# Kernel optimization log

Hardware: AMD Instinct MI355X
Metric: run time of the kernel (lower is better)

Reference implementation:

```python
import jax, jax.numpy as jnp
import numpy as np
import math

N = 4096
E = 131072
IN_DIM, HID, OUT = 512, 256, 64
DEPTH = 3
RATIO = 0.5


def setup_inputs() -> dict:
    key = jax.random.key(0)
    ks = jax.random.split(key, 12)

    def w(k, fi, fo):
        return jax.random.normal(k, (fi, fo), jnp.float32) * (1.0 / np.sqrt(fi).astype(np.float32))

    return {
        "x": jax.random.normal(ks[0], (N, IN_DIM), jnp.float32),
        "edge_index": jax.random.randint(ks[1], (2, E), 0, N, jnp.int32),
        "dW0": w(ks[2], IN_DIM, HID), "dW1": w(ks[3], HID, HID),
        "dW2": w(ks[4], HID, HID), "dW3": w(ks[5], HID, HID),
        "db0": jnp.zeros((HID,), jnp.float32), "db1": jnp.zeros((HID,), jnp.float32),
        "db2": jnp.zeros((HID,), jnp.float32), "db3": jnp.zeros((HID,), jnp.float32),
        "pw0": jax.random.normal(ks[6], (HID,), jnp.float32),
        "pw1": jax.random.normal(ks[7], (HID,), jnp.float32),
        "pw2": jax.random.normal(ks[8], (HID,), jnp.float32),
        "uW0": w(ks[9], HID, HID), "uW1": w(ks[10], HID, HID), "uW2": w(ks[11], HID, OUT),
        "ub0": jnp.zeros((HID,), jnp.float32), "ub1": jnp.zeros((HID,), jnp.float32),
        "ub2": jnp.zeros((OUT,), jnp.float32),
    }


def gcn_conv(x, A, W, b):
    # GCNConv(improved=True): A_hat = A + 2I, sym-normalized.
    n = A.shape[0]
    eye = jnp.eye(n, dtype=A.dtype)
    Ah = A + 2.0 * eye
    d = Ah.sum(axis=1)
    dinv = jnp.where(d > 0, jax.lax.rsqrt(d), 0.0)
    An = dinv[:, None] * Ah * dinv[None, :]
    return An @ (x @ W) + b


def augment_adj(A):
    # add self loops, square the (weighted) adjacency, remove self loops
    n = A.shape[0]
    eye = jnp.eye(n, dtype=A.dtype)
    Al = A + eye
    A2 = Al @ Al
    return A2 * (1.0 - eye)


def topk_pool(x, A, w, k):
    # TopKPooling: score = tanh(x.w/||w||); keep top-k; gate kept features by score.
    score = jnp.tanh((x @ w) / jnp.linalg.norm(w))
    _, perm = jax.lax.top_k(score, k)
    xp = x[perm] * score[perm][:, None]
    return xp, A[perm][:, perm], perm


def _forward(x, edge_index, down_Ws, down_bs, pool_ws, up_Ws, up_bs):
    A = jnp.zeros((N, N), jnp.float32).at[edge_index[0], edge_index[1]].set(1.0)
    x = jax.nn.relu(gcn_conv(x, A, down_Ws[0], down_bs[0]))
    xs, As, perms = [x], [A], []
    n = N
    for i in range(1, DEPTH + 1):
        A = augment_adj(A)
        k = int(math.ceil(RATIO * n)); n = k
        x, A, perm = topk_pool(x, A, pool_ws[i - 1], k)
        x = jax.nn.relu(gcn_conv(x, A, down_Ws[i], down_bs[i]))
        if i < DEPTH:
            xs.append(x); As.append(A)
        perms.append(perm)
    for i in range(DEPTH):
        j = DEPTH - 1 - i
        res, A, perm = xs[j], As[j], perms[j]
        up = jnp.zeros_like(res).at[perm].set(x)   # unpool (sum_res=True)
        x = res + up
        x = gcn_conv(x, A, up_Ws[i], up_bs[i])
        if i < DEPTH - 1:
            x = jax.nn.relu(x)
    return x


def reference(x, edge_index, dW0, dW1, dW2, dW3, db0, db1, db2, db3,
              pw0, pw1, pw2, uW0, uW1, uW2, ub0, ub1, ub2):
    return _forward(x, edge_index,
                    [dW0, dW1, dW2, dW3], [db0, db1, db2, db3],
                    [pw0, pw1, pw2],
                    [uW0, uW1, uW2], [ub0, ub1, ub2])
```

## Files before the change

kernel.cpp:

```cpp
#include <hip/hip_runtime.h>
#include <math.h>

#define NN 4096
#define EE 131072
#define IN_DIM 512
#define HID 256
#define OUT_DIM 64
#define ECAP 128

typedef __attribute__((ext_vector_type(8))) short bf8_t;
typedef __attribute__((ext_vector_type(4))) float f4_t;
typedef __attribute__((ext_vector_type(8))) unsigned short us8_t;
typedef __attribute__((ext_vector_type(4))) unsigned short us4_t;

#define GAS __attribute__((address_space(1)))
#define LAS __attribute__((address_space(3)))

__device__ __forceinline__ unsigned short f2bf(float v){
  union { float f; unsigned u; } x; x.f = v;
  unsigned r = x.u + 0x7fffu + ((x.u >> 16) & 1u);
  return (unsigned short)(r >> 16);
}
__device__ __forceinline__ float bf2f(unsigned short h){
  union { float f; unsigned u; } x; x.u = ((unsigned)h) << 16;
  return x.f;
}

__device__ __forceinline__ float waveReduceSum(float v){
#pragma unroll
  for (int off = 32; off > 0; off >>= 1) v += __shfl_down(v, off);
  return v;
}

__global__ __launch_bounds__(256) void k_prep(
    const float* __restrict__ x_in, const float* __restrict__ dW0,
    const float* __restrict__ dW1, const float* __restrict__ dW2,
    const float* __restrict__ dW3, const float* __restrict__ uW0,
    const float* __restrict__ uW1, const float* __restrict__ uW2,
    unsigned* __restrict__ bits,
    unsigned short* __restrict__ xinh, unsigned short* __restrict__ xinl,
    unsigned short* __restrict__ W0th, unsigned short* __restrict__ W0tl,
    unsigned short* __restrict__ W5th, unsigned short* __restrict__ W5tl,
    unsigned short* __restrict__ W2th, unsigned short* __restrict__ W2tl)
{
  int b = blockIdx.x;
  if (b < 128){
    int base = b * 4096 + threadIdx.x;
#pragma unroll
    for (int i = 0; i < 16; ++i) bits[base + i * 256] = 0;
    return;
  }
  b -= 128;
  if (b < 2048){
    int i0 = b * 1024 + threadIdx.x;
#pragma unroll
    for (int i = 0; i < 4; ++i){
      int idx = i0 + i * 256;
      float v = x_in[idx];
      unsigned short h = f2bf(v);
      xinh[idx] = h; xinl[idx] = f2bf(v - bf2f(h));
    }
    return;
  }
  b -= 2048;
  const float* X; unsigned short *Th, *Tl; int R, C, tile;
  if (b < 128){ X = dW0; Th = W0th; Tl = W0tl; R = 512; C = 256; tile = b; }
  else if (b < 448){
    int t2 = b - 128; int z = t2 >> 6; int rem = t2 & 63;
    const float* ws[5] = {dW1, dW2, dW3, uW0, uW1};
    X = ws[z]; Th = W5th + (size_t)z * 65536; Tl = W5tl + (size_t)z * 65536;
    R = 256; C = 256; tile = rem;
  } else { X = uW2; Th = W2th; Tl = W2tl; R = 256; C = 64; tile = b - 448; }
  int tpr = C >> 5;
  int bx = (tile % tpr) * 32, by = (tile / tpr) * 32;
  __shared__ float t[32][33];
  int tx = threadIdx.x & 31, ty = threadIdx.x >> 5;
#pragma unroll
  for (int i = 0; i < 4; ++i)
    t[ty + i * 8][tx] = X[(size_t)(by + ty + i * 8) * C + bx + tx];
  __syncthreads();
#pragma unroll
  for (int i = 0; i < 4; ++i){
    float v = t[tx][ty + i * 8];
    unsigned short h = f2bf(v);
    size_t o = (size_t)(bx + ty + i * 8) * R + by + tx;
    Th[o] = h; Tl[o] = f2bf(v - bf2f(h));
  }
}

__global__ void k_build_bits(const int* __restrict__ ei, unsigned* __restrict__ bits){
  int e = blockIdx.x * blockDim.x + threadIdx.x;
  if (e < EE){
    int r = ei[e], c = ei[EE + e];
    atomicOr(&bits[r * 128 + (c >> 5)], 1u << (c & 31));
  }
}

__global__ __launch_bounds__(128) void k_ell(const unsigned* __restrict__ bits,
                                             int* __restrict__ ell, int* __restrict__ cnt,
                                             float* __restrict__ dinv){
  int r = blockIdx.x, t = threadIdx.x;
  unsigned w = bits[r * 128 + t];
  int c = __popc(w);
  __shared__ int sc[128];
  sc[t] = c; __syncthreads();
  for (int off = 1; off < 128; off <<= 1){
    int a = sc[t], b = (t >= off) ? sc[t - off] : 0;
    __syncthreads(); sc[t] = a + b; __syncthreads();
  }
  int total = sc[127];
  int pos = sc[t] - c;
  int base = r * ECAP;
  while (w){
    int b = __ffs(w) - 1; w &= w - 1;
    if (pos < ECAP) ell[base + pos] = t * 32 + b;
    pos++;
  }
  if (t == 0){
    cnt[r] = (total < ECAP) ? total : ECAP;
    dinv[r] = 1.0f / sqrtf((float)total + 2.0f);
  }
}

template<int NCOLS, int RELU, int SC>
__global__ __launch_bounds__(256) void k_spmm_ell(
    const int* __restrict__ ell, const int* __restrict__ cnt,
    const float* __restrict__ Zs, const float* __restrict__ dinv,
    const float* __restrict__ bias, float* __restrict__ out,
    const float* __restrict__ scw, float* __restrict__ score)
{
  int r = blockIdx.x;
  __shared__ int s_idx[ECAP];
  __shared__ int s_n;
  __shared__ float sh[4 * NCOLS];
  __shared__ float sd[4], sq[4];
  if (threadIdx.x == 0) s_n = cnt[r];
  __syncthreads();
  int n = s_n; if (n > ECAP) n = ECAP;
  for (int i = threadIdx.x; i < n; i += 256) s_idx[i] = ell[r * ECAP + i];
  __syncthreads();
  int wv = threadIdx.x >> 6, lane = threadIdx.x & 63;
  if (NCOLS == 256){
    f4_t acc = (f4_t){0.f, 0.f, 0.f, 0.f};
    for (int e = wv; e < n; e += 4){
      const f4_t* row = (const f4_t*)(Zs + (size_t)s_idx[e] * 256);
      acc += row[lane];
    }
    ((f4_t*)(sh + wv * 256))[lane] = acc;
  } else {
    float acc = 0.f;
    for (int e = wv; e < n; e += 4)
      acc += Zs[(size_t)s_idx[e] * 64 + lane];
    sh[wv * 64 + lane] = acc;
  }
  __syncthreads();
  int t = threadIdx.x;
  float o = 0.f;
  if (t < NCOLS){
    float y = sh[t] + sh[NCOLS + t] + sh[2 * NCOLS + t] + sh[3 * NCOLS + t];
    float z = Zs[(size_t)r * NCOLS + t];
    o = dinv[r] * (y + 2.0f * z) + bias[t];
    if (RELU) o = fmaxf(o, 0.f);
    out[(size_t)r * NCOLS + t] = o;
  }
  if (SC){
    float w = scw[t];
    float d = waveReduceSum(o * w);
    float q = waveReduceSum(w * w);
    if (!lane){ sd[wv] = d; sq[wv] = q; }
    __syncthreads();
    if (!t) score[r] = tanhf((sd[0] + sd[1] + sd[2] + sd[3]) / sqrtf(sq[0] + sq[1] + sq[2] + sq[3]));
  }
}

__global__ __launch_bounds__(256) void k_pool_build(
    const float* __restrict__ x0, const float* __restrict__ score,
    const int* __restrict__ perm1, const int* __restrict__ inv1,
    const int* __restrict__ ell, const int* __restrict__ cnt,
    unsigned short* __restrict__ xph, unsigned short* __restrict__ xpl,
    unsigned short* __restrict__ Rb2,
    unsigned short* __restrict__ xu1h, unsigned short* __restrict__ xu1l)
{
  int b = blockIdx.x;
  if (b < 2048){
    int pr = perm1[b]; float s = score[pr];
    int c = threadIdx.x;
    float v = x0[(size_t)pr * 256 + c] * s;
    unsigned short h = f2bf(v);
    xph[(size_t)b * 256 + c] = h;
    xpl[(size_t)b * 256 + c] = f2bf(v - bf2f(h));
    return;
  }
  if (b < 6144){
    int k = b - 2048;
    __shared__ unsigned char row[2048];
    for (int i = threadIdx.x; i < 512; i += 256) ((int*)row)[i] = 0;
    __syncthreads();
    int n = cnt[k];
    for (int e = threadIdx.x; e < n; e += 256){
      int s = inv1[ell[k * ECAP + e]];
      if (s >= 0) row[s] = 1;
    }
    __syncthreads();
    if (threadIdx.x == 0){
      int sk = inv1[k];
      if (sk >= 0) row[sk] += 1;
    }
    __syncthreads();
    unsigned w = 0;
#pragma unroll
    for (int j = 0; j < 8; ++j) w |= ((unsigned)row[(threadIdx.x << 3) + j]) << (2 * j);
    Rb2[k * 256 + threadIdx.x] = (unsigned short)w;
    return;
  }
  int r = b - 6144;
  if (inv1[r] < 0){
    int c = threadIdx.x;
    float v = x0[(size_t)r * 256 + c];
    unsigned short h = f2bf(v);
    xu1h[(size_t)r * 256 + c] = h;
    xu1l[(size_t)r * 256 + c] = f2bf(v - bf2f(h));
  }
}

template<int SRCL, int OUTL>
__global__ __launch_bounds__(256) void k_pp(
    const float* __restrict__ x, const float* __restrict__ score,
    const int* __restrict__ perm, const int* __restrict__ inv, int n, int k,
    unsigned short* __restrict__ xph, unsigned short* __restrict__ xpl,
    unsigned short* __restrict__ xuh, unsigned short* __restrict__ xul,
    const unsigned short* __restrict__ Ah, const unsigned short* __restrict__ Al,
    unsigned short* __restrict__ Lh, unsigned short* __restrict__ Ll,
    unsigned short* __restrict__ Rh, unsigned short* __restrict__ Rl)
{
  __shared__ float t[32][33];
  __shared__ int sinv[32];
  int b = blockIdx.x, c = threadIdx.x;
  if (b < k){
    int pr = perm[b]; float s = score[pr];
    float v = x[(size_t)pr * 256 + c] * s;
    unsigned short h = f2bf(v);
    xph[(size_t)b * 256 + c] = h;
    xpl[(size_t)b * 256 + c] = f2bf(v - bf2f(h));
    return;
  }
  b -= k;
  if (b < n){
    if (inv[b] < 0){
      float v = x[(size_t)b * 256 + c];
      unsigned short h = f2bf(v);
      xuh[(size_t)b * 256 + c] = h;
      xul[(size_t)b * 256 + c] = f2bf(v - bf2f(h));
    }
    return;
  }
  b -= n;
  if (b < k){
    int r = b, pr = perm[r];
    for (int cc = threadIdx.x; cc < n; cc += 256){
      float v = bf2f(Ah[(size_t)pr * n + cc]);
      if (SRCL) v += bf2f(Al[(size_t)pr * n + cc]);
      if (pr == cc) v += 1.f;
      unsigned short h = f2bf(v);
      Lh[(size_t)r * n + cc] = h;
      if (OUTL) Ll[(size_t)r * n + cc] = f2bf(v - bf2f(h));
    }
    return;
  }
  b -= k;
  int tpr = n >> 5;
  int kt = b / tpr, ct = b - kt * tpr;
  int tx = threadIdx.x & 31, ty = threadIdx.x >> 5;
  if (threadIdx.x < 32) sinv[threadIdx.x] = inv[ct * 32 + threadIdx.x];
#pragma unroll
  for (int i = 0; i < 4; ++i){
    int kl = ty + i * 8;
    size_t src = (size_t)(kt * 32 + kl) * n + ct * 32 + tx;
    float v = bf2f(Ah[src]);
    if (SRCL) v += bf2f(Al[src]);
    t[kl][tx] = v;
  }
  __syncthreads();
#pragma unroll
  for (int i = 0; i < 4; ++i){
    int cl = ty + i * 8;
    int s = sinv[cl];
    if (s >= 0){
      float v = t[tx][cl];
      if (kt * 32 + tx == ct * 32 + cl) v += 1.f;
      unsigned short h = f2bf(v);
      size_t o = (size_t)s * n + kt * 32 + tx;
      Rh[o] = h;
      if (OUTL) Rl[o] = f2bf(v - bf2f(h));
    }
  }
}

__global__ __launch_bounds__(256) void k_sq1(const int* __restrict__ ell, const int* __restrict__ cnt,
                                             const int* __restrict__ perm,
                                             const unsigned short* __restrict__ Rb2,
                                             unsigned short* __restrict__ A1h,
                                             float* __restrict__ dinv1){
  int r = blockIdx.x;
  int pr = perm[r];
  __shared__ int s_idx[ECAP];
  __shared__ int s_n;
  __shared__ float sred[4];
  if (threadIdx.x == 0) s_n = cnt[pr];
  for (int i = threadIdx.x; i < ECAP; i += 256) s_idx[i] = ell[pr * ECAP + i];
  __syncthreads();
  int n = s_n; if (n > ECAP) n = ECAP;
  int colb = threadIdx.x * 8;
  auto expand = [](unsigned x) -> uint2 {
    uint2 e;
    e.x = (x & 3) | (((x >> 2) & 3) << 8) | (((x >> 4) & 3) << 16) | (((x >> 6) & 3) << 24);
    e.y = ((x >> 8) & 3) | (((x >> 10) & 3) << 8) | (((x >> 12) & 3) << 16) | (((x >> 14) & 3) << 24);
    return e;
  };
  uint2 acc = expand(Rb2[pr * 256 + threadIdx.x]);
  for (int e = 0; e < n; ++e){
    uint2 v = expand(Rb2[s_idx[e] * 256 + threadIdx.x]);
    acc.x += v.x; acc.y += v.y;
  }
  float fs = 0.f;
  us8_t o;
#pragma unroll
  for (int j = 0; j < 8; ++j){
    unsigned byte = ((j < 4 ? acc.x : acc.y) >> (8 * (j & 3))) & 0xFFu;
    if (colb + j == r) byte = 0;
    float f = (float)byte;
    fs += f;
    o[j] = f2bf(f);
  }
  *(us8_t*)(A1h + (size_t)r * 2048 + colb) = o;
  fs = waveReduceSum(fs);
  int lane = threadIdx.x & 63, wd = threadIdx.x >> 6;
  if (!lane) sred[wd] = fs;
  __syncthreads();
  if (!threadIdx.x)
    dinv1[r] = 1.0f / sqrtf(sred[0] + sred[1] + sred[2] + sred[3] + 2.0f);
}

template<int HAS_AL, int HAS_BL, int HAS_LL, int EPI>
__global__ __launch_bounds__(256) void k_mm(
    const unsigned short* __restrict__ Ah, const unsigned short* __restrict__ Al,
    const unsigned short* __restrict__ Bh, const unsigned short* __restrict__ Bl,
    int M, int N, int K, int KS, float* __restrict__ P,
    float* __restrict__ Cf, unsigned short* __restrict__ Ch, unsigned short* __restrict__ Cl,
    const float* __restrict__ dinv)
{
  constexpr int NARR = 2 + HAS_AL + HAS_BL;
  constexpr int BUF = NARR * 8192;
  __shared__ int4 ldsq[NARR * 512 * 2];
  char* ldsc = (char*)ldsq;

  const int tid = threadIdx.x, lane = tid & 63, wid = tid >> 6;
  const int wm = wid >> 1, wn = wid & 1;
  const int nbx = gridDim.x, nby = gridDim.y;
  const int tot = nbx * nby * gridDim.z;
  int id = blockIdx.x + nbx * (blockIdx.y + nby * blockIdx.z);
  if ((tot & 7) == 0) id = (id & 7) * (tot >> 3) + (id >> 3);
  const int sx = id % nbx; int remq = id / nbx;
  const int sy = remq % nby;
  const int bm = sy << 6, bn = sx << 6;
  const int z = remq / nby;
  const int l15 = lane & 15, l4 = lane >> 4;

  f4_t acc[2][2];
#pragma unroll
  for (int i = 0; i < 2; ++i)
#pragma unroll
    for (int j = 0; j < 2; ++j) acc[i][j] = (f4_t){0.f, 0.f, 0.f, 0.f};

  const size_t rb = (size_t)K * 2;
  const size_t kz = (size_t)z * KS * 2;
  const char* pAh = (const char*)Ah + (size_t)bm * rb;
  const char* pAl = HAS_AL ? (const char*)Al + (size_t)bm * rb : nullptr;
  const char* pBh = (const char*)Bh + (size_t)bn * rb;
  const char* pBl = HAS_BL ? (const char*)Bl + (size_t)bn * rb : nullptr;

  auto stage = [&](int t, int b2){
    char* ldsb = ldsc + b2 * BUF;
    const size_t kb = kz + (size_t)t * 128;
#pragma unroll
    for (int it = 0; it < 2; ++it){
      const int idx = tid + (it << 8);
      const int row = idx >> 3;
      const int kc = ((idx & 7) << 4) ^ ((row & 7) << 4);
      const size_t go = (size_t)row * rb + kb + kc;
      const int lo = idx * 16;
      __builtin_amdgcn_global_load_lds((const GAS void*)(pAh + go), (LAS void*)(ldsb + lo), 16, 0, 0);
      __builtin_amdgcn_global_load_lds((const GAS void*)(pBh + go), (LAS void*)(ldsb + 8192 + lo), 16, 0, 0);
      if (HAS_AL)
        __builtin_amdgcn_global_load_lds((const GAS void*)(pAl + go), (LAS void*)(ldsb + 16384 + lo), 16, 0, 0);
      if (HAS_BL)
        __builtin_amdgcn_global_load_lds((const GAS void*)(pBl + go), (LAS void*)(ldsb + (2 + HAS_AL) * 8192 + lo), 16, 0, 0);
    }
  };

  const int T = KS >> 6;
  stage(0, 0);
  int b = 0;
  for (int t = 0; t < T; ++t){
    if (t + 1 < T){
      stage(t + 1, b ^ 1);
      if constexpr (NARR == 2) asm volatile("s_waitcnt vmcnt(4)" ::: "memory");
      else if constexpr (NARR == 3) asm volatile("s_waitcnt vmcnt(6)" ::: "memory");
      else asm volatile("s_waitcnt vmcnt(8)" ::: "memory");
    } else {
      asm volatile("s_waitcnt vmcnt(0)" ::: "memory");
    }
    __syncthreads();
    const char* ldsb = ldsc + b * BUF;
#pragma unroll
    for (int ks = 0; ks < 2; ++ks){
      bf8_t aH[2], aL[2], bH[2], bL[2];
#pragma unroll
      for (int f = 0; f < 2; ++f){
        int ar = wm * 32 + f * 16 + l15;
        int aoff = ar * 128 + (((ks * 64) + (l4 << 4)) ^ ((ar & 7) << 4));
        aH[f] = *(const bf8_t*)(ldsb + aoff);
        if (HAS_AL) aL[f] = *(const bf8_t*)(ldsb + 16384 + aoff);
        int br = wn * 32 + f * 16 + l15;
        int boff = br * 128 + (((ks * 64) + (l4 << 4)) ^ ((br & 7) << 4));
        bH[f] = *(const bf8_t*)(ldsb + 8192 + boff);
        if (HAS_BL) bL[f] = *(const bf8_t*)(ldsb + (2 + HAS_AL) * 8192 + boff);
      }
#pragma unroll
      for (int i = 0; i < 2; ++i)
#pragma unroll
        for (int j = 0; j < 2; ++j){
          acc[i][j] = __builtin_amdgcn_mfma_f32_16x16x32_bf16(aH[i], bH[j], acc[i][j], 0, 0, 0);
          if (HAS_BL) acc[i][j] = __builtin_amdgcn_mfma_f32_16x16x32_bf16(aH[i], bL[j], acc[i][j], 0, 0, 0);
          if (HAS_AL) acc[i][j] = __builtin_amdgcn_mfma_f32_16x16x32_bf16(aL[i], bH[j], acc[i][j], 0, 0, 0);
          if (HAS_LL) acc[i][j] = __builtin_amdgcn_mfma_f32_16x16x32_bf16(aL[i], bL[j], acc[i][j], 0, 0, 0);
        }
    }
    __syncthreads();
    b ^= 1;
  }

  if (EPI == 4){
    float* LT = (float*)ldsc;
#pragma unroll
    for (int i = 0; i < 2; ++i)
#pragma unroll
      for (int j = 0; j < 2; ++j)
#pragma unroll
        for (int r = 0; r < 4; ++r){
          int lr = wm * 32 + i * 16 + l4 * 4 + r;
          int lc = wn * 32 + j * 16 + l15;
          float sv = dinv[bm + lr] * acc[i][j][r];
          Cf[(size_t)(bm + lr) * N + bn + lc] = sv;
          LT[lr * 68 + lc] = sv;
        }
    __syncthreads();
    int col = tid >> 2;
    int seg = (tid & 3) << 4;
    us8_t h0, h1, l0, l1;
#pragma unroll
    for (int mm = 0; mm < 8; ++mm){
      float v = LT[(seg + mm) * 68 + col];
      unsigned short h = f2bf(v);
      h0[mm] = h; l0[mm] = f2bf(v - bf2f(h));
    }
#pragma unroll
    for (int mm = 0; mm < 8; ++mm){
      float v = LT[(seg + 8 + mm) * 68 + col];
      unsigned short h = f2bf(v);
      h1[mm] = h; l1[mm] = f2bf(v - bf2f(h));
    }
    size_t ob = (size_t)(bn + col) * M + bm + seg;
    *(us8_t*)(Ch + ob) = h0;
    *(us8_t*)(Ch + ob + 8) = h1;
    *(us8_t*)(Cl + ob) = l0;
    *(us8_t*)(Cl + ob + 8) = l1;
    return;
  }

  float* Pz = (EPI == 0) ? P + (size_t)z * M * N : nullptr;
#pragma unroll
  for (int i = 0; i < 2; ++i)
#pragma unroll
    for (int j = 0; j < 2; ++j)
#pragma unroll
      for (int r = 0; r < 4; ++r){
        int grow = bm + wm * 32 + i * 16 + l4 * 4 + r;
        int gcol = bn + wn * 32 + j * 16 + l15;
        float v = acc[i][j][r];
        size_t o = (size_t)grow * N + gcol;
        if (EPI == 0){
          Pz[o] = v;
        } else {
          Cf[o] = dinv[grow] * v;
        }
      }
}

template<int EPI, int SC, int Z>
__global__ __launch_bounds__(256) void k_red(
    const float* __restrict__ P, int M, int NC,
    const float* __restrict__ dinv, const float* __restrict__ Zs,
    const float* __restrict__ bias,
    float* __restrict__ Of, unsigned short* __restrict__ Oh, unsigned short* __restrict__ Ol,
    float* __restrict__ dout, int relu,
    const float* __restrict__ scw, float* __restrict__ score,
    const float* __restrict__ res, const int* __restrict__ permsel)
{
  int w = threadIdx.x >> 6, lane = threadIdx.x & 63;
  int row = blockIdx.x * 4 + w;
  int prow = (EPI == 4) ? permsel[row] : 0;
  float di = (EPI != 3) ? dinv[row] : 0.f;
  float rsum = 0.f, o_d = 0.f, o_q = 0.f;
  for (int c0 = lane * 4; c0 < NC; c0 += 256){
    size_t o = (size_t)row * NC + c0;
    f4_t s = *(const f4_t*)(P + o);
#pragma unroll
    for (int zz = 1; zz < Z; ++zz) s += *(const f4_t*)(P + (size_t)zz * M * NC + o);
    if (EPI == 2){
      f4_t z4 = *(const f4_t*)(Zs + o);
      f4_t b4 = *(const f4_t*)(bias + c0);
      f4_t out;
#pragma unroll
      for (int j = 0; j < 4; ++j){
        float v = di * (s[j] + 2.0f * z4[j]) + b4[j];
        if (relu) v = fmaxf(v, 0.f);
        out[j] = v;
      }
      *(f4_t*)(Of + o) = out;
      if (SC){
        f4_t w4 = *(const f4_t*)(scw + c0);
#pragma unroll
        for (int j = 0; j < 4; ++j){ o_d += out[j] * w4[j]; o_q += w4[j] * w4[j]; }
      }
    } else if (EPI == 3){
      us4_t h4, l4v;
#pragma unroll
      for (int j = 0; j < 4; ++j){
        float v = (c0 + j == row) ? 0.f : s[j];
        unsigned short h = f2bf(v);
        h4[j] = h; l4v[j] = f2bf(v - bf2f(h));
        rsum += v;
      }
      *(us4_t*)(Oh + o) = h4;
      *(us4_t*)(Ol + o) = l4v;
    } else {
      f4_t z4 = *(const f4_t*)(Zs + o);
      f4_t b4 = *(const f4_t*)(bias + c0);
      f4_t r4 = *(const f4_t*)(res + (size_t)prow * NC + c0);
      us4_t h4, l4v;
#pragma unroll
      for (int j = 0; j < 4; ++j){
        float v = di * (s[j] + 2.0f * z4[j]) + b4[j];
        if (relu) v = fmaxf(v, 0.f);
        float comb = r4[j] + v;
        unsigned short h = f2bf(comb);
        h4[j] = h; l4v[j] = f2bf(comb - bf2f(h));
      }
      size_t od = (size_t)prow * NC + c0;
      *(us4_t*)(Oh + od) = h4;
      *(us4_t*)(Ol + od) = l4v;
    }
  }
  if (EPI == 3){
    rsum = waveReduceSum(rsum);
    if (!lane) dout[row] = 1.0f / sqrtf(rsum + 2.0f);
  }
  if (SC){
    o_d = waveReduceSum(o_d);
    o_q = waveReduceSum(o_q);
    if (!lane) score[row] = tanhf(o_d / sqrtf(o_q));
  }
}

__global__ void k_topk(const float* __restrict__ score, int n, int k,
                       int* __restrict__ perm, int* __restrict__ inv){
  int i = blockIdx.x; float si = score[i];
  int cnt = 0;
  for (int j = threadIdx.x; j < n; j += 256){
    float sj = score[j];
    if (sj > si || (sj == si && j < i)) cnt++;
  }
#pragma unroll
  for (int off = 32; off > 0; off >>= 1) cnt += __shfl_down(cnt, off);
  __shared__ int sh[4];
  int lane = threadIdx.x & 63, wid = threadIdx.x >> 6;
  if (lane == 0) sh[wid] = cnt;
  __syncthreads();
  if (threadIdx.x == 0){
    int rank = sh[0] + sh[1] + sh[2] + sh[3];
    if (rank < k){ perm[rank] = i; inv[i] = rank; }
    else inv[i] = -1;
  }
}

extern "C" void kernel_launch(void* const* d_in, const int* in_sizes, int n_in,
                              void* d_out, int out_size, void* d_ws, size_t ws_size,
                              hipStream_t stream){
  (void)in_sizes; (void)n_in; (void)out_size;
  const float* x_in = (const float*)d_in[0];
  const int*   ei   = (const int*)d_in[1];
  const float* dW0 = (const float*)d_in[2];
  const float* dW1 = (const float*)d_in[3];
  const float* dW2 = (const float*)d_in[4];
  const float* dW3 = (const float*)d_in[5];
  const float* db0 = (const float*)d_in[6];
  const float* db1 = (const float*)d_in[7];
  const float* db2 = (const float*)d_in[8];
  const float* db3 = (const float*)d_in[9];
  const float* pw0 = (const float*)d_in[10];
  const float* pw1 = (const float*)d_in[11];
  const float* pw2 = (const float*)d_in[12];
  const float* uW0 = (const float*)d_in[13];
  const float* uW1 = (const float*)d_in[14];
  const float* uW2 = (const float*)d_in[15];
  const float* ub0 = (const float*)d_in[16];
  const float* ub1 = (const float*)d_in[17];
  const float* ub2 = (const float*)d_in[18];

  char* p = (char*)d_ws;
  auto alloc = [&](size_t nbytes) -> void* {
    void* q = (void*)p; p += (nbytes + 255) & ~(size_t)255; return q;
  };
  unsigned* bits = (unsigned*)alloc((size_t)4096 * 128 * 4);
  int* ell = (int*)alloc((size_t)4096 * ECAP * 4);
  int* cnt = (int*)alloc(4096 * 4);
  int* inv1 = (int*)alloc(4096 * 4);
  int* inv2 = (int*)alloc(2048 * 4);
  int* inv3 = (int*)alloc(1024 * 4);
  unsigned short* Rb2 = (unsigned short*)alloc((size_t)4096 * 256 * 2);
  float* Pp = (float*)alloc((size_t)16 * 1024 * 1024);
  unsigned short* A1h = (unsigned short*)alloc((size_t)2048 * 2048 * 2);
  unsigned short* A2h = (unsigned short*)alloc((size_t)1024 * 1024 * 2);
  unsigned short* A2l = (unsigned short*)alloc((size_t)1024 * 1024 * 2);
  unsigned short* A3h = (unsigned short*)alloc((size_t)512 * 512 * 2);
  unsigned short* A3l = (unsigned short*)alloc((size_t)512 * 512 * 2);
  unsigned short* Lb2h = (unsigned short*)alloc((size_t)1024 * 2048 * 2);
  unsigned short* Rt2h = (unsigned short*)alloc((size_t)1024 * 2048 * 2);
  unsigned short* Lb3h = (unsigned short*)alloc((size_t)512 * 1024 * 2);
  unsigned short* Lb3l = (unsigned short*)alloc((size_t)512 * 1024 * 2);
  unsigned short* Rt3h = (unsigned short*)alloc((size_t)512 * 1024 * 2);
  unsigned short* Rt3l = (unsigned short*)alloc((size_t)512 * 1024 * 2);
  unsigned short* xinh = (unsigned short*)alloc((size_t)4096 * 512 * 2);
  unsigned short* xinl = (unsigned short*)alloc((size_t)4096 * 512 * 2);
  float* x0 = (float*)alloc((size_t)4096 * HID * 4);
  float* x1 = (float*)alloc((size_t)2048 * HID * 4);
  float* x2 = (float*)alloc((size_t)1024 * HID * 4);
  unsigned short* xu1h = (unsigned short*)alloc((size_t)4096 * HID * 2);
  unsigned short* xu1l = (unsigned short*)alloc((size_t)4096 * HID * 2);
  unsigned short* xu2h = (unsigned short*)alloc((size_t)2048 * HID * 2);
  unsigned short* xu2l = (unsigned short*)alloc((size_t)2048 * HID * 2);
  unsigned short* xu3h = (unsigned short*)alloc((size_t)1024 * HID * 2);
  unsigned short* xu3l = (unsigned short*)alloc((size_t)1024 * HID * 2);
  unsigned short* xph = (unsigned short*)alloc((size_t)2048 * HID * 2);
  unsigned short* xpl = (unsigned short*)alloc((size_t)2048 * HID * 2);
  unsigned short* W0th = (unsigned short*)alloc((size_t)256 * 512 * 2);
  unsigned short* W0tl = (unsigned short*)alloc((size_t)256 * 512 * 2);
  unsigned short* W5th = (unsigned short*)alloc((size_t)5 * 256 * 256 * 2);
  unsigned short* W5tl = (unsigned short*)alloc((size_t)5 * 256 * 256 * 2);
  unsigned short* W2th = (unsigned short*)alloc((size_t)64 * 256 * 2);
  unsigned short* W2tl = (unsigned short*)alloc((size_t)64 * 256 * 2);
  float* Zs  = (float*)alloc((size_t)4096 * HID * 4);
  unsigned short* ZsTh = (unsigned short*)alloc((size_t)256 * 2048 * 2);
  unsigned short* ZsTl = (unsigned short*)alloc((size_t)256 * 2048 * 2);
  float* dinv0 = (float*)alloc(4096 * 4);
  float* dinv1 = (float*)alloc(2048 * 4);
  float* dinv2 = (float*)alloc(1024 * 4);
  float* dinv3 = (float*)alloc(512 * 4);
  float* score = (float*)alloc(4096 * 4);
  int* perm1 = (int*)alloc(2048 * 4);
  int* perm2 = (int*)alloc(1024 * 4);
  int* perm3 = (int*)alloc(512 * 4);
  if ((size_t)(p - (char*)d_ws) > ws_size) return;

  k_prep<<<2640, 256, 0, stream>>>(x_in, dW0, dW1, dW2, dW3, uW0, uW1, uW2, bits,
                                   xinh, xinl, W0th, W0tl, W5th, W5tl, W2th, W2tl);
  k_build_bits<<<EE / 256, 256, 0, stream>>>(ei, bits);
  k_ell<<<4096, 128, 0, stream>>>(bits, ell, cnt, dinv0);

  { dim3 g(4, 64);
    k_mm<1,1,0,2><<<g, 256, 0, stream>>>(xinh, xinl, W0th, W0tl, 4096, HID, IN_DIM, IN_DIM,
                                         nullptr, Zs, nullptr, nullptr, dinv0); }
  k_spmm_ell<256,1,1><<<4096, 256, 0, stream>>>(ell, cnt, Zs, dinv0, db0, x0, pw0, score);

  k_topk<<<4096, 256, 0, stream>>>(score, 4096, 2048, perm1, inv1);
  k_pool_build<<<10240, 256, 0, stream>>>(x0, score, perm1, inv1, ell, cnt,
                                          xph, xpl, Rb2, xu1h, xu1l);
  k_sq1<<<2048, 256, 0, stream>>>(ell, cnt, perm1, Rb2, A1h, dinv1);
  { dim3 g(4, 32);
    k_mm<1,1,0,4><<<g, 256, 0, stream>>>(xph, xpl, W5th, W5tl, 2048, HID, HID, HID,
                                         nullptr, Zs, ZsTh, ZsTl, dinv1); }
  { dim3 g(4, 32, 4);
    k_mm<0,1,0,0><<<g, 256, 0, stream>>>(A1h, nullptr, ZsTh, ZsTl, 2048, HID, 2048, 512,
                                         Pp, nullptr, nullptr, nullptr, nullptr); }
  k_red<2,1,4><<<512, 256, 0, stream>>>(Pp, 2048, 256, dinv1, Zs, db1,
                                        x1, nullptr, nullptr, nullptr, 1, pw1, score, nullptr, nullptr);

  k_topk<<<2048, 256, 0, stream>>>(score, 2048, 1024, perm2, inv2);
  k_pp<0,0><<<8192, 256, 0, stream>>>(x1, score, perm2, inv2, 2048, 1024,
                                      xph, xpl, xu2h, xu2l, A1h, nullptr,
                                      Lb2h, nullptr, Rt2h, nullptr);
  { dim3 g(16, 16, 4);
    k_mm<0,0,0,0><<<g, 256, 0, stream>>>(Lb2h, nullptr, Rt2h, nullptr, 1024, 1024, 2048, 512,
                                         Pp, nullptr, nullptr, nullptr, nullptr); }
  k_red<3,0,4><<<256, 256, 0, stream>>>(Pp, 1024, 1024, nullptr, nullptr, nullptr,
                                        nullptr, A2h, A2l, dinv2, 0, nullptr, nullptr, nullptr, nullptr);
  { dim3 g(4, 16);
    k_mm<1,1,0,4><<<g, 256, 0, stream>>>(xph, xpl, W5th + 65536, W5tl + 65536, 1024, HID, HID, HID,
                                         nullptr, Zs, ZsTh, ZsTl, dinv2); }
  { dim3 g(4, 16, 4);
    k_mm<1,1,0,0><<<g, 256, 0, stream>>>(A2h, A2l, ZsTh, ZsTl, 1024, HID, 1024, 256,
                                         Pp, nullptr, nullptr, nullptr, nullptr); }
  k_red<2,1,4><<<256, 256, 0, stream>>>(Pp, 1024, 256, dinv2, Zs, db2,
                                        x2, nullptr, nullptr, nullptr, 1, pw2, score, nullptr, nullptr);

  k_topk<<<1024, 256, 0, stream>>>(score, 1024, 512, perm3, inv3);
  k_pp<1,1><<<3072, 256, 0, stream>>>(x2, score, perm3, inv3, 1024, 512,
                                      xph, xpl, xu3h, xu3l, A2h, A2l,
                                      Lb3h, Lb3l, Rt3h, Rt3l);
  { dim3 g(8, 8, 4);
    k_mm<1,1,1,0><<<g, 256, 0, stream>>>(Lb3h, Lb3l, Rt3h, Rt3l, 512, 512, 1024, 256,
                                         Pp, nullptr, nullptr, nullptr, nullptr); }
  k_red<3,0,4><<<128, 256, 0, stream>>>(Pp, 512, 512, nullptr, nullptr, nullptr,
                                        nullptr, A3h, A3l, dinv3, 0, nullptr, nullptr, nullptr, nullptr);
  { dim3 g(4, 8);
    k_mm<1,1,0,4><<<g, 256, 0, stream>>>(xph, xpl, W5th + 2 * 65536, W5tl + 2 * 65536, 512, HID, HID, HID,
                                         nullptr, Zs, ZsTh, ZsTl, dinv3); }
  { dim3 g(4, 8, 4);
    k_mm<1,1,0,0><<<g, 256, 0, stream>>>(A3h, A3l, ZsTh, ZsTl, 512, HID, 512, 128,
                                         Pp, nullptr, nullptr, nullptr, nullptr); }
  k_red<4,0,4><<<128, 256, 0, stream>>>(Pp, 512, 256, dinv3, Zs, db3,
                                        nullptr, xu3h, xu3l, nullptr, 1, nullptr, nullptr, x2, perm3);

  { dim3 g(4, 16);
    k_mm<1,1,0,4><<<g, 256, 0, stream>>>(xu3h, xu3l, W5th + 3 * 65536, W5tl + 3 * 65536, 1024, HID, HID, HID,
                                         nullptr, Zs, ZsTh, ZsTl, dinv2); }
  { dim3 g(4, 16, 4);
    k_mm<1,1,0,0><<<g, 256, 0, stream>>>(A2h, A2l, ZsTh, ZsTl, 1024, HID, 1024, 256,
                                         Pp, nullptr, nullptr, nullptr, nullptr); }
  k_red<4,0,4><<<256, 256, 0, stream>>>(Pp, 1024, 256, dinv2, Zs, ub0,
                                        nullptr, xu2h, xu2l, nullptr, 1, nullptr, nullptr, x1, perm2);

  { dim3 g(4, 32);
    k_mm<1,1,0,4><<<g, 256, 0, stream>>>(xu2h, xu2l, W5th + 4 * 65536, W5tl + 4 * 65536, 2048, HID, HID, HID,
                                         nullptr, Zs, ZsTh, ZsTl, dinv1); }
  { dim3 g(4, 32, 4);
    k_mm<0,1,0,0><<<g, 256, 0, stream>>>(A1h, nullptr, ZsTh, ZsTl, 2048, HID, 2048, 512,
                                         Pp, nullptr, nullptr, nullptr, nullptr); }
  k_red<4,0,4><<<512, 256, 0, stream>>>(Pp, 2048, 256, dinv1, Zs, ub1,
                                        nullptr, xu1h, xu1l, nullptr, 1, nullptr, nullptr, x0, perm1);

  { dim3 g(1, 64);
    k_mm<1,1,0,2><<<g, 256, 0, stream>>>(xu1h, xu1l, W2th, W2tl, 4096, OUT_DIM, HID, HID,
                                         nullptr, Zs, nullptr, nullptr, dinv0); }
  k_spmm_ell<64,0,0><<<4096, 256, 0, stream>>>(ell, cnt, Zs, dinv0, ub2, (float*)d_out, nullptr, nullptr);
}
```

Baseline: 224.9 us.

## Fuse edge bitmap build with first GEMM and move dinv scaling into SpMM

The first feature GEMM no longer needs dinv0, so it can run in the same launch as the edge-bitmap atomics. A combined kernel dispatches 512 blocks to set bitmap bits and 256 blocks to the GEMM, which now writes unscaled output. The first SpMM then applies the per-neighbor dinv on the fly from a shared-memory cache and scales the self term. This removes one launch and overlaps the atomic pass with the matmul, at the cost of an extra dinv gather and multiply per edge in the SpMM.

```diff
diff --git a/kernel.cpp b/kernel.cpp
--- a/kernel.cpp
+++ b/kernel.cpp
@@ -88,14 +88,6 @@
   }
 }
 
-__global__ void k_build_bits(const int* __restrict__ ei, unsigned* __restrict__ bits){
-  int e = blockIdx.x * blockDim.x + threadIdx.x;
-  if (e < EE){
-    int r = ei[e], c = ei[EE + e];
-    atomicOr(&bits[r * 128 + (c >> 5)], 1u << (c & 31));
-  }
-}
-
 __global__ __launch_bounds__(128) void k_ell(const unsigned* __restrict__ bits,
                                              int* __restrict__ ell, int* __restrict__ cnt,
                                              float* __restrict__ dinv){
@@ -122,7 +114,7 @@
   }
 }
 
-template<int NCOLS, int RELU, int SC>
+template<int NCOLS, int RELU, int SC, int DS>
 __global__ __launch_bounds__(256) void k_spmm_ell(
     const int* __restrict__ ell, const int* __restrict__ cnt,
     const float* __restrict__ Zs, const float* __restrict__ dinv,
@@ -131,26 +123,35 @@
 {
   int r = blockIdx.x;
   __shared__ int s_idx[ECAP];
+  __shared__ float s_dv[ECAP];
   __shared__ int s_n;
   __shared__ float sh[4 * NCOLS];
   __shared__ float sd[4], sq[4];
   if (threadIdx.x == 0) s_n = cnt[r];
   __syncthreads();
   int n = s_n; if (n > ECAP) n = ECAP;
-  for (int i = threadIdx.x; i < n; i += 256) s_idx[i] = ell[r * ECAP + i];
+  for (int i = threadIdx.x; i < n; i += 256){
+    int idx = ell[r * ECAP + i];
+    s_idx[i] = idx;
+    if (DS) s_dv[i] = dinv[idx];
+  }
   __syncthreads();
   int wv = threadIdx.x >> 6, lane = threadIdx.x & 63;
   if (NCOLS == 256){
     f4_t acc = (f4_t){0.f, 0.f, 0.f, 0.f};
     for (int e = wv; e < n; e += 4){
-      const f4_t* row = (const f4_t*)(Zs + (size_t)s_idx[e] * 256);
-      acc += row[lane];
+      f4_t row = ((const f4_t*)(Zs + (size_t)s_idx[e] * 256))[lane];
+      if (DS) row *= s_dv[e];
+      acc += row;
     }
     ((f4_t*)(sh + wv * 256))[lane] = acc;
   } else {
     float acc = 0.f;
-    for (int e = wv; e < n; e += 4)
-      acc += Zs[(size_t)s_idx[e] * 64 + lane];
+    for (int e = wv; e < n; e += 4){
+      float v = Zs[(size_t)s_idx[e] * 64 + lane];
+      if (DS) v *= s_dv[e];
+      acc += v;
+    }
     sh[wv * 64 + lane] = acc;
   }
   __syncthreads();
@@ -158,8 +159,10 @@
   float o = 0.f;
   if (t < NCOLS){
     float y = sh[t] + sh[NCOLS + t] + sh[2 * NCOLS + t] + sh[3 * NCOLS + t];
+    float di = dinv[r];
     float z = Zs[(size_t)r * NCOLS + t];
-    o = dinv[r] * (y + 2.0f * z) + bias[t];
+    if (DS) z = di * z;
+    o = di * (y + 2.0f * z) + bias[t];
     if (RELU) o = fmaxf(o, 0.f);
     out[(size_t)r * NCOLS + t] = o;
   }
@@ -342,7 +345,7 @@
 }
 
 template<int HAS_AL, int HAS_BL, int HAS_LL, int EPI>
-__global__ __launch_bounds__(256) void k_mm(
+__device__ __forceinline__ void mm_body(char* ldsc, int id, int nbx, int nby, int tot,
     const unsigned short* __restrict__ Ah, const unsigned short* __restrict__ Al,
     const unsigned short* __restrict__ Bh, const unsigned short* __restrict__ Bl,
     int M, int N, int K, int KS, float* __restrict__ P,
@@ -351,14 +354,9 @@
 {
   constexpr int NARR = 2 + HAS_AL + HAS_BL;
   constexpr int BUF = NARR * 8192;
-  __shared__ int4 ldsq[NARR * 512 * 2];
-  char* ldsc = (char*)ldsq;
 
   const int tid = threadIdx.x, lane = tid & 63, wid = tid >> 6;
   const int wm = wid >> 1, wn = wid & 1;
-  const int nbx = gridDim.x, nby = gridDim.y;
-  const int tot = nbx * nby * gridDim.z;
-  int id = blockIdx.x + nbx * (blockIdx.y + nby * blockIdx.z);
   if ((tot & 7) == 0) id = (id & 7) * (tot >> 3) + (id >> 3);
   const int sx = id % nbx; int remq = id / nbx;
   const int sy = remq % nby;
@@ -491,10 +489,48 @@
         size_t o = (size_t)grow * N + gcol;
         if (EPI == 0){
           Pz[o] = v;
+        } else if (EPI == 2){
+          Cf[o] = dinv[grow] * v;
         } else {
-          Cf[o] = dinv[grow] * v;
+          Cf[o] = v;
         }
       }
+}
+
+template<int HAS_AL, int HAS_BL, int HAS_LL, int EPI>
+__global__ __launch_bounds__(256) void k_mm(
+    const unsigned short* __restrict__ Ah, const unsigned short* __restrict__ Al,
+    const unsigned short* __restrict__ Bh, const unsigned short* __restrict__ Bl,
+    int M, int N, int K, int KS, float* __restrict__ P,
+    float* __restrict__ Cf, unsigned short* __restrict__ Ch, unsigned short* __restrict__ Cl,
+    const float* __restrict__ dinv)
+{
+  constexpr int NARR = 2 + HAS_AL + HAS_BL;
+  __shared__ int4 ldsq[NARR * 512 * 2];
+  const int nbx = gridDim.x, nby = gridDim.y;
+  const int tot = nbx * nby * gridDim.z;
+  int id = blockIdx.x + nbx * (blockIdx.y + nby * blockIdx.z);
+  mm_body<HAS_AL, HAS_BL, HAS_LL, EPI>((char*)ldsq, id, nbx, nby, tot,
+      Ah, Al, Bh, Bl, M, N, K, KS, P, Cf, Ch, Cl, dinv);
+}
+
+__global__ __launch_bounds__(256) void k_fuse0(
+    const int* __restrict__ ei, unsigned* __restrict__ bits,
+    const unsigned short* __restrict__ Ah, const unsigned short* __restrict__ Al,
+    const unsigned short* __restrict__ Bh, const unsigned short* __restrict__ Bl,
+    float* __restrict__ Cf)
+{
+  __shared__ int4 ldsq[4 * 512 * 2];
+  if (blockIdx.x < 512){
+    int e = blockIdx.x * 256 + threadIdx.x;
+    int r = ei[e], c = ei[EE + e];
+    atomicOr(&bits[r * 128 + (c >> 5)], 1u << (c & 31));
+    return;
+  }
+  int id = blockIdx.x - 512;
+  mm_body<1,1,0,5>((char*)ldsq, id, 4, 64, 256,
+      Ah, Al, Bh, Bl, 4096, HID, IN_DIM, IN_DIM,
+      nullptr, Cf, nullptr, nullptr, nullptr);
 }
 
 template<int EPI, int SC, int Z>
@@ -675,13 +711,9 @@
 
   k_prep<<<2640, 256, 0, stream>>>(x_in, dW0, dW1, dW2, dW3, uW0, uW1, uW2, bits,
                                    xinh, xinl, W0th, W0tl, W5th, W5tl, W2th, W2tl);
-  k_build_bits<<<EE / 256, 256, 0, stream>>>(ei, bits);
+  k_fuse0<<<768, 256, 0, stream>>>(ei, bits, xinh, xinl, W0th, W0tl, Zs);
   k_ell<<<4096, 128, 0, stream>>>(bits, ell, cnt, dinv0);
-
-  { dim3 g(4, 64);
-    k_mm<1,1,0,2><<<g, 256, 0, stream>>>(xinh, xinl, W0th, W0tl, 4096, HID, IN_DIM, IN_DIM,
-                                         nullptr, Zs, nullptr, nullptr, dinv0); }
-  k_spmm_ell<256,1,1><<<4096, 256, 0, stream>>>(ell, cnt, Zs, dinv0, db0, x0, pw0, score);
+  k_spmm_ell<256,1,1,1><<<4096, 256, 0, stream>>>(ell, cnt, Zs, dinv0, db0, x0, pw0, score);
 
   k_topk<<<4096, 256, 0, stream>>>(score, 4096, 2048, perm1, inv1);
   k_pool_build<<<10240, 256, 0, stream>>>(x0, score, perm1, inv1, ell, cnt,
@@ -753,5 +785,5 @@
   { dim3 g(1, 64);
     k_mm<1,1,0,2><<<g, 256, 0, stream>>>(xu1h, xu1l, W2th, W2tl, 4096, OUT_DIM, HID, HID,
                                          nullptr, Zs, nullptr, nullptr, dinv0); }
-  k_spmm_ell<64,0,0><<<4096, 256, 0, stream>>>(ell, cnt, Zs, dinv0, ub2, (float*)d_out, nullptr, nullptr);
-}
+  k_spmm_ell<64,0,0,0><<<4096, 256, 0, stream>>>(ell, cnt, Zs, dinv0, ub2, (float*)d_out, nullptr, nullptr);
+}
```

After: 222.7 us, median of 2. About the same (-1.0%).
